# Performance work log

Hardware: AMD Instinct MI355X
Metric: run time of the kernel (lower is better)

## Reference

```python
import jax, jax.numpy as jnp
import numpy as np


def setup_inputs() -> dict:
    key = jax.random.key(0)
    k1, k2 = jax.random.split(key)
    inputs = jax.random.normal(k1, (16, 4096, 512), dtype=jnp.float32)
    # torch init is uniform(-1/num_codes, 1/num_codes); match scale
    codebooks = jax.random.uniform(k2, (4, 1024, 512), dtype=jnp.float32,
                                   minval=-1.0 / 1024, maxval=1.0 / 1024)
    return {"inputs": inputs, "codebooks": codebooks}


def _vq_level(flat, codebook):
    # flat: [N, D], codebook: [K, D]
    dists = (jnp.sum(flat * flat, axis=1, keepdims=True)
             + jnp.sum(codebook * codebook, axis=1)
             - 2.0 * jnp.matmul(flat, codebook.T))  # [N, K]
    idx = jnp.argmin(dists, axis=1)                  # [N]
    quantized = codebook[idx]                         # [N, D]
    return quantized, idx


def reference(inputs, codebooks):
    sg = jax.lax.stop_gradient
    num_levels = codebooks.shape[0]
    shp = inputs.shape
    D = shp[-1]
    flat_in = inputs.reshape(-1, D)

    residual = flat_in
    total_q = jnp.zeros_like(flat_in)
    all_idx = []
    total_q_loss = jnp.float32(0.0)
    total_e_loss = jnp.float32(0.0)
    for lvl in range(num_levels):
        quantized, idx = _vq_level(residual, codebooks[lvl])
        q_loss = jnp.mean((quantized - sg(residual)) ** 2)
        e_loss = jnp.mean((sg(quantized) - residual) ** 2)
        all_idx.append(idx.reshape(shp[:-1]))
        total_q = total_q + quantized
        total_q_loss = total_q_loss + q_loss
        total_e_loss = total_e_loss + e_loss
        residual = residual - sg(quantized)

    total_q = total_q.reshape(shp)
    final_ste = inputs + sg(total_q - inputs)
    return (final_ste,
            total_q_loss / num_levels,
            total_e_loss / num_levels,
            jnp.stack(all_idx, axis=0))
```

## Files before the change

kernel.cpp:

```cpp
#include <hip/hip_runtime.h>


#define NROWS 65536
#define DDIM  512
#define KC    1024

#define AS1 __attribute__((address_space(1)))
#define AS3 __attribute__((address_space(3)))

typedef __attribute__((ext_vector_type(8))) short short8v;
typedef __attribute__((ext_vector_type(4))) float f32x4;

__device__ __forceinline__ unsigned short f2bf(float f) {
  unsigned u = __float_as_uint(f);
  unsigned r = (u + 0x7FFFu + ((u >> 16) & 1u)) >> 16;
  return (unsigned short)r;
}

__device__ __forceinline__ bool lexlt(float v1, int i1, float v2, int i2) {
  return (v1 < v2) || (v1 == v2 && i1 < i2);
}

__device__ __forceinline__ void merge3(float& v0, float& v1, float& v2,
                                       float m0, float m1, float m2) {
  float x1 = fmaxf(v0, m0); v0 = fminf(v0, m0);
  float y = fminf(v1, m1), z = fmaxf(v1, m1);
  float nv1 = fminf(x1, y);
  v2 = fminf(fmaxf(x1, y), fminf(z, fminf(v2, m2)));
  v1 = nv1;
}

__device__ __forceinline__ void top3of4(float k0, float k1, float k2, float k3,
                                        float& m0, float& m1, float& m2) {
  float a = fminf(k0, k1), b = fmaxf(k0, k1);
  float c = fminf(k2, k3), d = fmaxf(k2, k3);
  m0 = fminf(a, c);
  float f = fmaxf(a, c), g = fminf(b, d);
  m1 = fminf(f, g); m2 = fmaxf(f, g);
}

__device__ __forceinline__ void wg_barrier() {
  asm volatile("" ::: "memory");
  __builtin_amdgcn_s_barrier();
  asm volatile("" ::: "memory");
}

__global__ void __launch_bounds__(256)
prep_kernel(const float* __restrict__ cbs, float* __restrict__ cn32,
            const float4* __restrict__ x4, ushort4* __restrict__ cbb4,
            ushort4* __restrict__ res4) {
  const int code = blockIdx.x;
  const int l = threadIdx.x;
  if (l < 32) {
    const int b = l >> 3, j = l & 7;
    const float* p = cbs + (size_t)code * DDIM + b * 128 + j;
    float racc;
    {
      #pragma clang fp contract(off)
      float x0 = p[0];
      racc = x0 * x0;
      for (int s = 1; s < 16; ++s) { float x = p[8 * s]; float sq = x * x; racc = racc + sq; }
    }
    {
      #pragma clang fp contract(off)
      float o;
      o = __shfl_xor(racc, 1, 64);  racc = racc + o;
      o = __shfl_xor(racc, 2, 64);  racc = racc + o;
      o = __shfl_xor(racc, 4, 64);  racc = racc + o;
      o = __shfl_xor(racc, 8, 64);  racc = racc + o;
      o = __shfl_xor(racc, 16, 64); racc = racc + o;
      if (l == 0) cn32[code] = racc;
    }
  }
  const float4* cb4 = (const float4*)cbs;
  for (long i = blockIdx.x * 256L + threadIdx.x; i < 524288L;
       i += (long)gridDim.x * 256) {
    float4 v = cb4[i];
    ushort4 o; o.x = f2bf(v.x); o.y = f2bf(v.y); o.z = f2bf(v.z); o.w = f2bf(v.w);
    cbb4[i] = o;
  }
  for (long i = blockIdx.x * 256L + threadIdx.x; i < 8388608L;
       i += (long)gridDim.x * 256) {
    float4 v = x4[i];
    ushort4 o; o.x = f2bf(v.x); o.y = f2bf(v.y); o.z = f2bf(v.z); o.w = f2bf(v.w);
    res4[i] = o;
  }
}

__global__ void __launch_bounds__(256)
resupd_kernel(const float4* __restrict__ x4, const float* __restrict__ cbs,
              const float* __restrict__ idx_f, ushort4* __restrict__ res4,
              int nlev) {
  const int gwave = (blockIdx.x * 256 + threadIdx.x) >> 6;
  const int lane  = threadIdx.x & 63;
  const int nwaves = gridDim.x * 4;
  const float4* cb4 = (const float4*)cbs;
  for (int row = gwave; row < NROWS; row += nwaves) {
    int ci[4];
    for (int l = 0; l < nlev; ++l) ci[l] = (int)idx_f[(size_t)l * NROWS + row];
    #pragma unroll
    for (int half = 0; half < 2; ++half) {
      const int p = half * 64 + lane;
      float4 v = x4[(size_t)row * 128 + p];
      for (int l = 0; l < nlev; ++l) {
        const float4 c = cb4[((size_t)(l * KC + ci[l])) * 128 + p];
        v.x -= c.x; v.y -= c.y; v.z -= c.z; v.w -= c.w;
      }
      ushort4 o; o.x = f2bf(v.x); o.y = f2bf(v.y); o.z = f2bf(v.z); o.w = f2bf(v.w);
      res4[(size_t)row * 128 + p] = o;
    }
  }
}

template <int LVL>
__global__ void __launch_bounds__(256, 4)
score_gemm(const ushort* __restrict__ res, const ushort* __restrict__ cbb,
           const float* __restrict__ cn32, float* __restrict__ partials) {
  __shared__ ushort lds[16384];

  const int t = threadIdx.x;
  const int w = t >> 6, lane = t & 63;
  const int fr = lane & 15, kg = lane >> 4;
  const int rh = w >> 1, ch = w & 1;
  const int xcd = blockIdx.x & 7;
  const int j   = blockIdx.x >> 3;
  const int colTile = j & 7;
  const int rowTile = xcd * 64 + (j >> 3);
  const int row0 = rowTile * 128;

  const ushort* Asrc = res + (size_t)row0 * DDIM;
  const ushort* Bsrc = cbb + ((size_t)LVL * KC + colTile * 128) * DDIM;

  const int r0s = t >> 2, kq = t & 3;
  const int r1s = 64 + r0s;
  const int swz = (t >> 3) & 3;
  const size_t off0 = (size_t)r0s * DDIM + (size_t)((kq ^ swz) * 8);
  const size_t off1 = (size_t)r1s * DDIM + (size_t)((kq ^ swz) * 8);
  const int kgs = (kg ^ ((fr >> 1) & 3)) * 8;

  f32x4 acc[4][4];
  #pragma unroll
  for (int ri = 0; ri < 4; ++ri)
    #pragma unroll
    for (int ci = 0; ci < 4; ++ci) { f32x4 z = {0.f, 0.f, 0.f, 0.f}; acc[ri][ci] = z; }

#define STG(KS, BI)                                                           \
  do {                                                                        \
    __builtin_amdgcn_global_load_lds(                                         \
        (const AS1 unsigned*)(Asrc + off0 + (KS) * 32),                       \
        (AS3 unsigned*)&lds[(BI) * 4096 + w * 512], 16, 0, 0);                \
    __builtin_amdgcn_global_load_lds(                                         \
        (const AS1 unsigned*)(Asrc + off1 + (KS) * 32),                       \
        (AS3 unsigned*)&lds[(BI) * 4096 + 2048 + w * 512], 16, 0, 0);         \
    __builtin_amdgcn_global_load_lds(                                         \
        (const AS1 unsigned*)(Bsrc + off0 + (KS) * 32),                       \
        (AS3 unsigned*)&lds[8192 + (BI) * 4096 + w * 512], 16, 0, 0);         \
    __builtin_amdgcn_global_load_lds(                                         \
        (const AS1 unsigned*)(Bsrc + off1 + (KS) * 32),                       \
        (AS3 unsigned*)&lds[8192 + (BI) * 4096 + 2048 + w * 512], 16, 0, 0);  \
  } while (0)

  STG(0, 0);
  #pragma unroll
  for (int ks = 0; ks < 16; ++ks) {
    const int cur = ks & 1;
    if (ks < 15) {
      STG(ks + 1, !cur);
      asm volatile("s_waitcnt vmcnt(4)" ::: "memory");
    } else {
      asm volatile("s_waitcnt vmcnt(0)" ::: "memory");
    }
    wg_barrier();
    short8v a[4], b[4];
    #pragma unroll
    for (int i = 0; i < 4; ++i)
      a[i] = *(const short8v*)&lds[cur * 4096 + (rh * 64 + i * 16 + fr) * 32 + kgs];
    #pragma unroll
    for (int i = 0; i < 4; ++i)
      b[i] = *(const short8v*)&lds[8192 + cur * 4096 + (ch * 64 + i * 16 + fr) * 32 + kgs];
    __builtin_amdgcn_s_setprio(1);
    #pragma unroll
    for (int ri = 0; ri < 4; ++ri)
      #pragma unroll
      for (int ci = 0; ci < 4; ++ci)
        acc[ri][ci] = __builtin_amdgcn_mfma_f32_16x16x32_bf16(
            a[ri], b[ci], acc[ri][ci], 0, 0, 0);
    __builtin_amdgcn_s_setprio(0);
    wg_barrier();
  }
#undef STG

  float* hT = (float*)lds;
  float cnv[4];
  #pragma unroll
  for (int ci = 0; ci < 4; ++ci)
    cnv[ci] = cn32[LVL * KC + colTile * 128 + ch * 64 + ci * 16 + fr] + 0.25f;

  #pragma unroll
  for (int ri = 0; ri < 4; ++ri) {
    #pragma unroll
    for (int j2 = 0; j2 < 4; ++j2) {
      float k[4];
      #pragma unroll
      for (int ci = 0; ci < 4; ++ci) {
        float s = fmaf(-2.0f, acc[ri][ci][j2], cnv[ci]);
        unsigned col = (unsigned)(colTile * 128 + ch * 64 + ci * 16 + fr);
        unsigned u = (__float_as_uint(s) & 0xFFFFFC00u) | col;
        k[ci] = __uint_as_float(u);
      }
      float m0, m1, m2;
      top3of4(k[0], k[1], k[2], k[3], m0, m1, m2);
      #pragma unroll
      for (int m = 1; m <= 8; m <<= 1) {
        float t0 = __shfl_xor(m0, m, 64);
        float t1 = __shfl_xor(m1, m, 64);
        float t2 = __shfl_xor(m2, m, 64);
        merge3(m0, m1, m2, t0, t1, t2);
      }
      if (fr == 0) {
        int row64 = ri * 16 + kg * 4 + j2;
        hT[(((rh * 2 + ch) * 64) + row64) * 3 + 0] = m0;
        hT[(((rh * 2 + ch) * 64) + row64) * 3 + 1] = m1;
        hT[(((rh * 2 + ch) * 64) + row64) * 3 + 2] = m2;
      }
    }
  }
  __syncthreads();

  if (t < 128) {
    const int lrh = t >> 6, r64 = t & 63;
    float u0 = hT[(((lrh * 2 + 0) * 64) + r64) * 3 + 0];
    float u1 = hT[(((lrh * 2 + 0) * 64) + r64) * 3 + 1];
    float u2 = hT[(((lrh * 2 + 0) * 64) + r64) * 3 + 2];
    float s0 = hT[(((lrh * 2 + 1) * 64) + r64) * 3 + 0];
    float s1 = hT[(((lrh * 2 + 1) * 64) + r64) * 3 + 1];
    float s2 = hT[(((lrh * 2 + 1) * 64) + r64) * 3 + 2];
    merge3(u0, u1, u2, s0, s1, s2);
    const int grow = row0 + lrh * 64 + r64;
    partials[(size_t)(colTile * 3 + 0) * NROWS + grow] = u0;
    partials[(size_t)(colTile * 3 + 1) * NROWS + grow] = u1;
    partials[(size_t)(colTile * 3 + 2) * NROWS + grow] = u2;
  }
}

template <int LVL>
__global__ void __launch_bounds__(256)
post_kernel(const float* __restrict__ partials, const float* __restrict__ x,
            const float* __restrict__ cbs, const float* __restrict__ cn32,
            float* __restrict__ idx_io) {
  __shared__ int qlist[256];
  __shared__ int qcL[256][4];
  __shared__ int qn_l;
  const int t = threadIdx.x;
  if (t == 0) qn_l = 0;
  __syncthreads();

  const int row = blockIdx.x * 256 + t;
  {
    float v0 = 3.4e38f, v1 = 3.4e38f, v2 = 3.4e38f, v3 = 3.4e38f;
    #pragma unroll
    for (int p = 0; p < 24; ++p) {
      const float kv = partials[(size_t)p * NROWS + row];
      const bool b3 = kv < v3, b2 = kv < v2, b1 = kv < v1, b0 = kv < v0;
      v3 = b3 ? (b2 ? v2 : kv) : v3;
      v2 = b2 ? (b1 ? v1 : kv) : v2;
      v1 = b1 ? (b0 ? v0 : kv) : v1;
      v0 = b0 ? kv : v0;
    }
    if (v1 - v0 > 1e-3f) {
      idx_io[(size_t)LVL * NROWS + row] = (float)(__float_as_uint(v0) & 1023u);
    } else {
      int pos = atomicAdd(&qn_l, 1);
      qlist[pos] = row;
      qcL[pos][0] = (int)(__float_as_uint(v0) & 1023u);
      qcL[pos][1] = (int)(__float_as_uint(v1) & 1023u);
      qcL[pos][2] = (int)(__float_as_uint(v2) & 1023u);
      qcL[pos][3] = (int)(__float_as_uint(v3) & 1023u);
    }
  }
  __syncthreads();

  const int qn = qn_l;
  const float4* x4  = (const float4*)x;
  const float4* cb4 = (const float4*)cbs;
  const float*  cnL = cn32 + LVL * KC;

  for (int base = 0; base < qn * 4; base += 256) {
    const int wi = base + t;
    if (wi < qn * 4) {
      const int qi = wi >> 2, cd = wi & 3;
      const int grow = qlist[qi];
      const int ci   = qcL[qi][cd];
      const float4* xr = x4 + (size_t)grow * 128;
      const float4* cq = cb4 + ((size_t)LVL * KC + ci) * 128;
      const float4* cl[LVL > 0 ? LVL : 1];
      #pragma unroll
      for (int l = 0; l < LVL; ++l)
        cl[l] = cb4 +
                ((size_t)(l * KC + (int)idx_io[(size_t)l * NROWS + grow])) * 128;

      float Bk[4];
      float dacc = 0.0f;
      #pragma unroll
      for (int b = 0; b < 4; ++b) {
        #pragma clang fp contract(off)
        float racc[8];
        for (int s = 0; s < 16; ++s) {
          const int q = b * 32 + s * 2;
          float4 v0 = xr[q], v1 = xr[q + 1];
          #pragma unroll
          for (int l = 0; l < LVL; ++l) {
            const float4 c0 = cl[l][q], c1 = cl[l][q + 1];
            v0.x -= c0.x; v0.y -= c0.y; v0.z -= c0.z; v0.w -= c0.w;
            v1.x -= c1.x; v1.y -= c1.y; v1.z -= c1.z; v1.w -= c1.w;
          }
          if (s == 0) {
            racc[0] = v0.x * v0.x; racc[1] = v0.y * v0.y;
            racc[2] = v0.z * v0.z; racc[3] = v0.w * v0.w;
            racc[4] = v1.x * v1.x; racc[5] = v1.y * v1.y;
            racc[6] = v1.z * v1.z; racc[7] = v1.w * v1.w;
          } else {
            float sq;
            sq = v0.x * v0.x; racc[0] = racc[0] + sq;
            sq = v0.y * v0.y; racc[1] = racc[1] + sq;
            sq = v0.z * v0.z; racc[2] = racc[2] + sq;
            sq = v0.w * v0.w; racc[3] = racc[3] + sq;
            sq = v1.x * v1.x; racc[4] = racc[4] + sq;
            sq = v1.y * v1.y; racc[5] = racc[5] + sq;
            sq = v1.z * v1.z; racc[6] = racc[6] + sq;
            sq = v1.w * v1.w; racc[7] = racc[7] + sq;
          }
          const float4 c0 = cq[q], c1 = cq[q + 1];
          dacc = fmaf(v0.x, c0.x, dacc); dacc = fmaf(v0.y, c0.y, dacc);
          dacc = fmaf(v0.z, c0.z, dacc); dacc = fmaf(v0.w, c0.w, dacc);
          dacc = fmaf(v1.x, c1.x, dacc); dacc = fmaf(v1.y, c1.y, dacc);
          dacc = fmaf(v1.z, c1.z, dacc); dacc = fmaf(v1.w, c1.w, dacc);
        }
        float t0 = (racc[0] + racc[1]) + (racc[2] + racc[3]);
        float t1 = (racc[4] + racc[5]) + (racc[6] + racc[7]);
        Bk[b] = t0 + t1;
      }
      float vfin;
      {
        #pragma clang fp contract(off)
        float Arow = (Bk[0] + Bk[1]) + (Bk[2] + Bk[3]);
        float ab = Arow + cnL[ci];
        vfin = ab - 2.0f * dacc;
      }
      float bv = vfin; int bi = ci;
      float ov = __shfl_xor(bv, 1, 64); int oi = __shfl_xor(bi, 1, 64);
      if (lexlt(ov, oi, bv, bi)) { bv = ov; bi = oi; }
      ov = __shfl_xor(bv, 2, 64); oi = __shfl_xor(bi, 2, 64);
      if (lexlt(ov, oi, bv, bi)) { bv = ov; bi = oi; }
      if (cd == 0) idx_io[(size_t)LVL * NROWS + grow] = (float)bi;
    }
  }
}

__global__ void __launch_bounds__(256)
finalize_kernel(const float4* __restrict__ x4, const float* __restrict__ cbs,
                const float* __restrict__ idx_f, float4* __restrict__ out,
                double* __restrict__ loss_acc) {
  double ls0 = 0.0, ls1 = 0.0, ls2 = 0.0, ls3 = 0.0;
  const int gwave = (blockIdx.x * 256 + threadIdx.x) >> 6;
  const int lane  = threadIdx.x & 63;
  const int nwaves = gridDim.x * 4;
  const float4* cb4 = (const float4*)cbs;

  for (int row = gwave; row < NROWS; row += nwaves) {
    int ci[4];
    #pragma unroll
    for (int l = 0; l < 4; ++l) ci[l] = (int)idx_f[(size_t)l * NROWS + row];
    #pragma unroll
    for (int half = 0; half < 2; ++half) {
      const int p = half * 64 + lane;
      const float4 xv = x4[(size_t)row * 128 + p];
      float4 rr = xv;
      float4 tq = make_float4(0.f, 0.f, 0.f, 0.f);
      #pragma unroll
      for (int l = 0; l < 4; ++l) {
        const float4 qv = cb4[((size_t)(l * KC + ci[l])) * 128 + p];
        rr.x -= qv.x; rr.y -= qv.y; rr.z -= qv.z; rr.w -= qv.w;
        const double ss = (double)rr.x * rr.x + (double)rr.y * rr.y +
                          (double)rr.z * rr.z + (double)rr.w * rr.w;
        if      (l == 0) ls0 += ss;
        else if (l == 1) ls1 += ss;
        else if (l == 2) ls2 += ss;
        else             ls3 += ss;
        tq.x += qv.x; tq.y += qv.y; tq.z += qv.z; tq.w += qv.w;
      }
      float4 o;
      o.x = xv.x + (tq.x - xv.x);
      o.y = xv.y + (tq.y - xv.y);
      o.z = xv.z + (tq.z - xv.z);
      o.w = xv.w + (tq.w - xv.w);
      out[(size_t)row * 128 + p] = o;
    }
  }
  #pragma unroll
  for (int m = 1; m <= 32; m <<= 1) {
    ls0 += __shfl_xor(ls0, m, 64);
    ls1 += __shfl_xor(ls1, m, 64);
    ls2 += __shfl_xor(ls2, m, 64);
    ls3 += __shfl_xor(ls3, m, 64);
  }
  __shared__ double sred[4][4];
  const int wave = threadIdx.x >> 6;
  if ((threadIdx.x & 63) == 0) {
    sred[wave][0] = ls0; sred[wave][1] = ls1; sred[wave][2] = ls2; sred[wave][3] = ls3;
  }
  __syncthreads();
  if (threadIdx.x < 4) {
    const double v = sred[0][threadIdx.x] + sred[1][threadIdx.x] +
                     sred[2][threadIdx.x] + sred[3][threadIdx.x];
    atomicAdd(loss_acc + threadIdx.x, v);
  }
}

__global__ void write_losses_kernel(const double* __restrict__ loss_acc,
                                    float* __restrict__ out) {
  if (threadIdx.x == 0 && blockIdx.x == 0) {
    const double inv = 1.0 / (double)((size_t)NROWS * (size_t)DDIM);
    const double tv = (loss_acc[0] * inv + loss_acc[1] * inv +
                       loss_acc[2] * inv + loss_acc[3] * inv) * 0.25;
    out[33554432] = (float)tv;
    out[33554433] = (float)tv;
  }
}

extern "C" void kernel_launch(void* const* d_in, const int* in_sizes, int n_in,
                              void* d_out, int out_size, void* d_ws, size_t ws_size,
                              hipStream_t stream) {
  (void)in_sizes; (void)n_in; (void)out_size; (void)ws_size;
  const float* x   = (const float*)d_in[0];
  const float* cbs = (const float*)d_in[1];
  float* out_f     = (float*)d_out;
  float* idx_f     = out_f + 33554434;

  ushort* cbb  = (ushort*)d_ws;
  ushort* res  = (ushort*)((char*)d_ws + 4194304);
  float*  cn32 = (float*)((char*)d_ws + 4194304 + 67108864);
  double* loss = (double*)((char*)d_ws + 4194304 + 67108864 + 16384);

  float* partials = out_f;

  hipMemsetAsync(loss, 0, 4 * sizeof(double), stream);

  prep_kernel<<<4096, 256, 0, stream>>>(cbs, cn32, (const float4*)x,
                                        (ushort4*)cbb, (ushort4*)res);

  score_gemm<0><<<4096, 256, 0, stream>>>(res, cbb, cn32, partials);
  post_kernel<0><<<256, 256, 0, stream>>>(partials, x, cbs, cn32, idx_f);
  resupd_kernel<<<2048, 256, 0, stream>>>((const float4*)x, cbs, idx_f,
                                          (ushort4*)res, 1);

  score_gemm<1><<<4096, 256, 0, stream>>>(res, cbb, cn32, partials);
  post_kernel<1><<<256, 256, 0, stream>>>(partials, x, cbs, cn32, idx_f);
  resupd_kernel<<<2048, 256, 0, stream>>>((const float4*)x, cbs, idx_f,
                                          (ushort4*)res, 2);

  score_gemm<2><<<4096, 256, 0, stream>>>(res, cbb, cn32, partials);
  post_kernel<2><<<256, 256, 0, stream>>>(partials, x, cbs, cn32, idx_f);
  resupd_kernel<<<2048, 256, 0, stream>>>((const float4*)x, cbs, idx_f,
                                          (ushort4*)res, 3);

  score_gemm<3><<<4096, 256, 0, stream>>>(res, cbb, cn32, partials);
  post_kernel<3><<<256, 256, 0, stream>>>(partials, x, cbs, cn32, idx_f);

  finalize_kernel<<<2048, 256, 0, stream>>>((const float4*)x, cbs, idx_f,
                                            (float4*)d_out, loss);
  write_losses_kernel<<<1, 64, 0, stream>>>(loss, out_f);
}
```

Measured before the change: 909.4 us.

## Fuse residual update into post kernel and shrink rows per block

Removes the separate residual-update kernel and performs the bf16 residual rewrite at the end of each level's post kernel, using the chosen index held in shared memory. Each block now handles 32 rows instead of 256, and the grid grows to 2048 blocks, so the ambiguous-candidate rescoring is spread across more blocks and runs without the serial loop. This saves a launch and one pass over the index array per level. In exchange, only 32 of the 256 threads do the top-4 selection, and the rescoring path assumes at most 64 ambiguous rows per block, which holds because a block has only 32 rows.

```diff
diff --git a/kernel.cpp b/kernel.cpp
--- a/kernel.cpp
+++ b/kernel.cpp
@@ -87,31 +87,6 @@
   }
 }
 
-__global__ void __launch_bounds__(256)
-resupd_kernel(const float4* __restrict__ x4, const float* __restrict__ cbs,
-              const float* __restrict__ idx_f, ushort4* __restrict__ res4,
-              int nlev) {
-  const int gwave = (blockIdx.x * 256 + threadIdx.x) >> 6;
-  const int lane  = threadIdx.x & 63;
-  const int nwaves = gridDim.x * 4;
-  const float4* cb4 = (const float4*)cbs;
-  for (int row = gwave; row < NROWS; row += nwaves) {
-    int ci[4];
-    for (int l = 0; l < nlev; ++l) ci[l] = (int)idx_f[(size_t)l * NROWS + row];
-    #pragma unroll
-    for (int half = 0; half < 2; ++half) {
-      const int p = half * 64 + lane;
-      float4 v = x4[(size_t)row * 128 + p];
-      for (int l = 0; l < nlev; ++l) {
-        const float4 c = cb4[((size_t)(l * KC + ci[l])) * 128 + p];
-        v.x -= c.x; v.y -= c.y; v.z -= c.z; v.w -= c.w;
-      }
-      ushort4 o; o.x = f2bf(v.x); o.y = f2bf(v.y); o.z = f2bf(v.z); o.w = f2bf(v.w);
-      res4[(size_t)row * 128 + p] = o;
-    }
-  }
-}
-
 template <int LVL>
 __global__ void __launch_bounds__(256, 4)
 score_gemm(const ushort* __restrict__ res, const ushort* __restrict__ cbb,
@@ -247,16 +222,18 @@
 __global__ void __launch_bounds__(256)
 post_kernel(const float* __restrict__ partials, const float* __restrict__ x,
             const float* __restrict__ cbs, const float* __restrict__ cn32,
-            float* __restrict__ idx_io) {
-  __shared__ int qlist[256];
-  __shared__ int qcL[256][4];
+            float* __restrict__ idx_io, ushort4* __restrict__ res4) {
+  __shared__ int qlist[32];
+  __shared__ int qcL[32][4];
+  __shared__ int idxL[32];
   __shared__ int qn_l;
   const int t = threadIdx.x;
+  const int row0 = blockIdx.x * 32;
   if (t == 0) qn_l = 0;
   __syncthreads();
 
-  const int row = blockIdx.x * 256 + t;
-  {
+  if (t < 32) {
+    const int row = row0 + t;
     float v0 = 3.4e38f, v1 = 3.4e38f, v2 = 3.4e38f, v3 = 3.4e38f;
     #pragma unroll
     for (int p = 0; p < 24; ++p) {
@@ -268,10 +245,12 @@
       v0 = b0 ? kv : v0;
     }
     if (v1 - v0 > 1e-3f) {
-      idx_io[(size_t)LVL * NROWS + row] = (float)(__float_as_uint(v0) & 1023u);
+      const int bi = (int)(__float_as_uint(v0) & 1023u);
+      idx_io[(size_t)LVL * NROWS + row] = (float)bi;
+      idxL[t] = bi;
     } else {
       int pos = atomicAdd(&qn_l, 1);
-      qlist[pos] = row;
+      qlist[pos] = t;
       qcL[pos][0] = (int)(__float_as_uint(v0) & 1023u);
       qcL[pos][1] = (int)(__float_as_uint(v1) & 1023u);
       qcL[pos][2] = (int)(__float_as_uint(v2) & 1023u);
@@ -283,13 +262,12 @@
   const int qn = qn_l;
   const float4* x4  = (const float4*)x;
   const float4* cb4 = (const float4*)cbs;
-  const float*  cnL = cn32 + LVL * KC;
-
-  for (int base = 0; base < qn * 4; base += 256) {
-    const int wi = base + t;
-    if (wi < qn * 4) {
-      const int qi = wi >> 2, cd = wi & 3;
-      const int grow = qlist[qi];
+  {
+    const float* cnL = cn32 + LVL * KC;
+    if (t < qn * 4) {
+      const int qi = t >> 2, cd = t & 3;
+      const int lrow = qlist[qi];
+      const int grow = row0 + lrow;
       const int ci   = qcL[qi][cd];
       const float4* xr = x4 + (size_t)grow * 128;
       const float4* cq = cb4 + ((size_t)LVL * KC + ci) * 128;
@@ -352,7 +330,37 @@
       if (lexlt(ov, oi, bv, bi)) { bv = ov; bi = oi; }
       ov = __shfl_xor(bv, 2, 64); oi = __shfl_xor(bi, 2, 64);
       if (lexlt(ov, oi, bv, bi)) { bv = ov; bi = oi; }
-      if (cd == 0) idx_io[(size_t)LVL * NROWS + grow] = (float)bi;
+      if (cd == 0) {
+        idx_io[(size_t)LVL * NROWS + grow] = (float)bi;
+        idxL[lrow] = bi;
+      }
+    }
+  }
+  __syncthreads();
+
+  if constexpr (LVL < 3) {
+    const int wave = t >> 6, lane = t & 63;
+    #pragma unroll
+    for (int r = 0; r < 8; ++r) {
+      const int lrow = wave * 8 + r;
+      const int row = row0 + lrow;
+      int ci[4];
+      #pragma unroll
+      for (int l = 0; l < LVL; ++l)
+        ci[l] = (int)idx_io[(size_t)l * NROWS + row];
+      ci[LVL] = idxL[lrow];
+      #pragma unroll
+      for (int half = 0; half < 2; ++half) {
+        const int p = half * 64 + lane;
+        float4 v = x4[(size_t)row * 128 + p];
+        #pragma unroll
+        for (int l = 0; l <= LVL; ++l) {
+          const float4 c = cb4[((size_t)(l * KC + ci[l])) * 128 + p];
+          v.x -= c.x; v.y -= c.y; v.z -= c.z; v.w -= c.w;
+        }
+        ushort4 o; o.x = f2bf(v.x); o.y = f2bf(v.y); o.z = f2bf(v.z); o.w = f2bf(v.w);
+        res4[(size_t)row * 128 + p] = o;
+      }
     }
   }
 }
@@ -450,22 +458,20 @@
                                         (ushort4*)cbb, (ushort4*)res);
 
   score_gemm<0><<<4096, 256, 0, stream>>>(res, cbb, cn32, partials);
-  post_kernel<0><<<256, 256, 0, stream>>>(partials, x, cbs, cn32, idx_f);
-  resupd_kernel<<<2048, 256, 0, stream>>>((const float4*)x, cbs, idx_f,
-                                          (ushort4*)res, 1);
+  post_kernel<0><<<2048, 256, 0, stream>>>(partials, x, cbs, cn32, idx_f,
+                                           (ushort4*)res);
 
   score_gemm<1><<<4096, 256, 0, stream>>>(res, cbb, cn32, partials);
-  post_kernel<1><<<256, 256, 0, stream>>>(partials, x, cbs, cn32, idx_f);
-  resupd_kernel<<<2048, 256, 0, stream>>>((const float4*)x, cbs, idx_f,
-                                          (ushort4*)res, 2);
+  post_kernel<1><<<2048, 256, 0, stream>>>(partials, x, cbs, cn32, idx_f,
+                                           (ushort4*)res);
 
   score_gemm<2><<<4096, 256, 0, stream>>>(res, cbb, cn32, partials);
-  post_kernel<2><<<256, 256, 0, stream>>>(partials, x, cbs, cn32, idx_f);
-  resupd_kernel<<<2048, 256, 0, stream>>>((const float4*)x, cbs, idx_f,
-                                          (ushort4*)res, 3);
+  post_kernel<2><<<2048, 256, 0, stream>>>(partials, x, cbs, cn32, idx_f,
+                                           (ushort4*)res);
 
   score_gemm<3><<<4096, 256, 0, stream>>>(res, cbb, cn32, partials);
-  post_kernel<3><<<256, 256, 0, stream>>>(partials, x, cbs, cn32, idx_f);
+  post_kernel<3><<<2048, 256, 0, stream>>>(partials, x, cbs, cn32, idx_f,
+                                           (ushort4*)res);
 
   finalize_kernel<<<2048, 256, 0, stream>>>((const float4*)x, cbs, idx_f,
                                             (float4*)d_out, loss);
```

Measured after the change: 1.167 ms. 1.28x slower.
